# Kernel optimization log

Measured on AMD Instinct MI355X. Metric: run time of the kernel, lower is better.

## Reference

```python
import jax, jax.numpy as jnp
import numpy as np

N = 50_000        # nodes
E = 1_600_000     # edges (avg degree 32)
H = 64            # hidden_channels
DEPTH = 3         # -> 2*DEPTH mid conv layers


def setup_inputs() -> dict:
    key = jax.random.key(0)
    ks = jax.random.split(key, 8)
    x = jax.random.normal(ks[0], (N, 1), dtype=jnp.float32)
    edge_index = jax.random.randint(ks[1], (2, E), 0, N, dtype=jnp.int32)
    s = 0.1  # small init scale
    W_in = s * jax.random.normal(ks[2], (2 * 1 + 1, H), dtype=jnp.float32)
    b_in = jnp.zeros((H,), jnp.float32)
    W_mid = s * jax.random.normal(ks[3], (2 * DEPTH, 2 * H + 1, H), dtype=jnp.float32)
    b_mid = jnp.zeros((2 * DEPTH, H), jnp.float32)
    W_out = s * jax.random.normal(ks[4], (2 * H + 1, 1), dtype=jnp.float32)
    b_out = jnp.zeros((1,), jnp.float32)
    return {"x": x, "edge_index": edge_index, "W_in": W_in, "b_in": b_in,
            "W_mid": W_mid, "b_mid": b_mid, "W_out": W_out, "b_out": b_out}


def _conv(x, src, dst, sign, inv_deg, W, b):
    """Directional_EdgeConv: mean_{j->i} Linear([x_i, x_j - x_i, sign(j-i)])."""
    x_i = x[dst]                                   # [E, F] target feats
    x_j = x[src]                                   # [E, F] source feats
    feat = jnp.concatenate([x_i, x_j - x_i, sign], axis=-1)  # [E, 2F+1]
    msg = feat @ W + b                             # [E, out]
    agg = jax.ops.segment_sum(msg, dst, num_segments=x.shape[0])  # [N, out]
    return agg * inv_deg                           # mean aggregation


def reference(x, edge_index, W_in, b_in, W_mid, b_mid, W_out, b_out):
    src = edge_index[0]
    dst = edge_index[1]
    # vectorized replacement of the per-edge Python sign loop
    sign = jnp.sign((src - dst).astype(x.dtype))[:, None]        # [E, 1]
    deg = jax.ops.segment_sum(jnp.ones((src.shape[0],), x.dtype), dst,
                              num_segments=x.shape[0])
    inv_deg = (1.0 / jnp.maximum(deg, 1.0))[:, None]             # [N, 1]

    x2 = _conv(x, src, dst, sign, inv_deg, W_in, b_in)
    for l in range(DEPTH):
        x1 = jax.nn.leaky_relu(
            _conv(x2, src, dst, sign, inv_deg, W_mid[2 * l], b_mid[2 * l]))
        x2 = jax.nn.leaky_relu(
            _conv(x1, src, dst, sign, inv_deg, W_mid[2 * l + 1], b_mid[2 * l + 1]) + x2)
    return _conv(x2, src, dst, sign, inv_deg, W_out, b_out) + x
```

## Files before the change

kernel.cpp:

```cpp
#include <hip/hip_runtime.h>
#include <hip/hip_fp16.h>

#define HDIM 64
#define NEG_SLOPE 0.01f
#define CAPB 8192
#define BCAP 6144

typedef _Float16 half8 __attribute__((ext_vector_type(8)));
typedef float f32x4 __attribute__((ext_vector_type(4)));

static __device__ __forceinline__ float h_lo(unsigned d) {
    return __half2float(__ushort_as_half((unsigned short)(d & 0xffffu)));
}
static __device__ __forceinline__ float h_hi(unsigned d) {
    return __half2float(__ushort_as_half((unsigned short)(d >> 16)));
}
static __device__ __forceinline__ unsigned packh(float a, float b) {
    unsigned short ra = __half_as_ushort(__float2half(a));
    unsigned short rb = __half_as_ushort(__float2half(b));
    return ((unsigned)rb << 16) | (unsigned)ra;
}
static __device__ __forceinline__ half8 u4h(uint4 v) {
    union { uint4 u; half8 h; } x; x.u = v; return x.h;
}
static __device__ __forceinline__ __half2 uh2(unsigned u) {
    union { unsigned u; __half2 h; } x; x.u = u; return x.h;
}
static __device__ __forceinline__ unsigned h2u(__half2 h) {
    union { __half2 h; unsigned u; } x; x.h = h; return x.u;
}
static __device__ __forceinline__ __half2 hsum8(unsigned a, unsigned b, unsigned c, unsigned d,
                                                unsigned e, unsigned f, unsigned g, unsigned h) {
    __half2 p0 = __hadd2(uh2(a), uh2(b));
    __half2 p1 = __hadd2(uh2(c), uh2(d));
    __half2 p2 = __hadd2(uh2(e), uh2(f));
    __half2 p3 = __hadd2(uh2(g), uh2(h));
    return __hadd2(__hadd2(p0, p1), __hadd2(p2, p3));
}

__global__ void k_setup(int ptotal, const float* __restrict__ W_mid,
                        unsigned short* __restrict__ WTh,
                        int NB, int* gcur, int N, unsigned* xAP, unsigned* xBP) {
    int i = blockIdx.x * blockDim.x + threadIdx.x;
    if (i < ptotal) {
        int l = i >> 13;
        int rem = i & 8191;
        int h = rem >> 7;
        int k = rem & 127;
        const float* W = W_mid + (size_t)l * 129 * 64;
        float v = W[k * 64 + h] - ((k < 64) ? W[(64 + k) * 64 + h] : 0.f);
        WTh[i] = __half_as_ushort(__float2half(v));
    }
    if (i < NB) gcur[i] = i * CAPB;
    if (i < 32) xAP[(size_t)N * 32 + i] = 0u;
    else if (i < 64) xBP[(size_t)N * 32 + (i - 32)] = 0u;
}

__global__ void k_bucket(int E, const int* __restrict__ src, const int* __restrict__ dst,
                         int* gcur, unsigned* __restrict__ bucketed, int NB) {
    __shared__ int lh[512];
    __shared__ int lbase[512];
    int t = threadIdx.x;
    int e0 = blockIdx.x * 2048;
    for (int i = t; i < NB; i += 256) lh[i] = 0;
    __syncthreads();
    int dv[8];
#pragma unroll
    for (int k = 0; k < 8; ++k) {
        int e = e0 + k * 256 + t;
        dv[k] = (e < E) ? dst[e] : -1;
    }
#pragma unroll
    for (int k = 0; k < 8; ++k)
        if (dv[k] >= 0) atomicAdd(&lh[((unsigned)dv[k]) >> 7], 1);
    __syncthreads();
    for (int i = t; i < NB; i += 256) {
        int c = lh[i];
        lbase[i] = (c > 0) ? atomicAdd(&gcur[i], c) : 0;
        lh[i] = 0;
    }
    __syncthreads();
    int sv[8];
#pragma unroll
    for (int k = 0; k < 8; ++k) {
        int e = e0 + k * 256 + t;
        sv[k] = (e < E) ? src[e] : 0;
    }
#pragma unroll
    for (int k = 0; k < 8; ++k) {
        if (dv[k] >= 0) {
            int b = ((unsigned)dv[k]) >> 7;
            int r = atomicAdd(&lh[b], 1);
            int pos = lbase[b] + r;
            if (pos < (b + 1) * CAPB)
                bucketed[pos] = ((unsigned)dv[k] << 16) | (unsigned)sv[k];
        }
    }
}

__global__ void k_bktscan(int NB, int N, const int* __restrict__ gcur,
                          int* gstart, int* rowptr) {
    __shared__ int sd[512];
    int t = threadIdx.x;
    int c = (t < NB) ? min(gcur[t] - t * CAPB, CAPB) : 0;
    sd[t] = c;
    __syncthreads();
    int x = c;
    for (int s = 1; s < 512; s <<= 1) {
        int p = (t >= s) ? sd[t - s] : 0;
        __syncthreads();
        x += p;
        sd[t] = x;
        __syncthreads();
    }
    if (t < NB) gstart[t] = x - c;
    if (t == NB - 1) {
        gstart[NB] = x;
        rowptr[N] = x;
    }
}

__global__ void k_csr(int N, const unsigned* __restrict__ bucketed, const int* __restrict__ gcur,
                      const int* __restrict__ gstart, unsigned short* __restrict__ csr,
                      unsigned short* __restrict__ pcsr,
                      int* __restrict__ rowptr, float* __restrict__ ssinv) {
    __shared__ unsigned st[BCAP];
    __shared__ int hist[128], cur[128], excl[128], sgp[128];
    int b = blockIdx.x, t = threadIdx.x;
    int n0 = b << 7;
    int nn = min(128, N - n0);
    int cnt = min(gcur[b] - b * CAPB, CAPB);
    int base = gstart[b];
    if (t < 128) { hist[t] = 0; sgp[t] = 0; }
    unsigned sent = ((unsigned)N << 16) | (unsigned)N;
    unsigned* pb32 = (unsigned*)(pcsr + ((size_t)b << 13));
    for (int i = t; i < 4096; i += 256) pb32[i] = sent;
    __syncthreads();
    bool single = (cnt <= BCAP);
    for (int off = 0; off < cnt; off += BCAP) {
        int bs = min(BCAP, cnt - off);
        for (int i = t; i < bs; i += 256) {
            unsigned w = bucketed[b * CAPB + off + i];
            if (single) st[i] = w;
            int d = (int)(w >> 16);
            int s = (int)(w & 0xffffu);
            int dl = d - n0;
            atomicAdd(&hist[dl], 1);
            atomicAdd(&sgp[dl], ((s < d) ? 1024 : 0) + ((s == d) ? 1 : 0));
        }
    }
    __syncthreads();
    int deg_t = (t < 128) ? hist[t] : 0;
    int x = deg_t;
    for (int s = 1; s < 128; s <<= 1) {
        int p = (t < 128 && t >= s) ? hist[t - s] : 0;
        __syncthreads();
        if (t < 128) { x += p; hist[t] = x; }
        __syncthreads();
    }
    if (t < 128) {
        int ex = hist[t] - deg_t;
        excl[t] = ex;
        cur[t] = ex;
        if (t < nn) {
            rowptr[n0 + t] = base + ex;
            int sg = sgp[t];
            int lt = sg >> 10, eq = sg & 1023;
            float ss = (float)(deg_t - eq - 2 * lt);
            ssinv[n0 + t] = (deg_t > 0) ? ss / (float)deg_t : 0.f;
        }
    }
    __syncthreads();
    for (int off = 0; off < cnt; off += BCAP) {
        int bs = min(BCAP, cnt - off);
        if (!single) {
            for (int i = t; i < bs; i += 256) st[i] = bucketed[b * CAPB + off + i];
            __syncthreads();
        }
        for (int i = t; i < bs; i += 256) {
            unsigned w = st[i];
            int dl = (int)(w >> 16) - n0;
            unsigned short sval = (unsigned short)(w & 0xffffu);
            int p = atomicAdd(&cur[dl], 1);
            csr[base + p] = sval;
            int r = p - excl[dl];
            if (r < 64) pcsr[((size_t)(n0 + dl) << 6) + r] = sval;
        }
        if (!single) __syncthreads();
    }
}

__global__ void k_in(int N, const float* __restrict__ x0,
                     const int* __restrict__ rowptr, const unsigned short* __restrict__ csr,
                     const float* __restrict__ ssinv,
                     const float* __restrict__ W_in, const float* __restrict__ b_in,
                     unsigned* __restrict__ xoutP) {
    int wid = blockIdx.x * (blockDim.x >> 6) + (threadIdx.x >> 6);
    int lane = threadIdx.x & 63;
    if (wid >= N) return;
    int beg = rowptr[wid], end = rowptr[wid + 1];
    int deg = end - beg;
    float s = 0.f;
    for (int e = beg + lane; e < end; e += 64) s += x0[csr[e]];
    for (int m = 32; m >= 1; m >>= 1) s += __shfl_xor(s, m, 64);
    float invd = 1.f / (float)max(deg, 1);
    float mean = s * invd;
    float xi = x0[wid];
    float w1 = W_in[lane], w2 = W_in[64 + lane], w3 = W_in[128 + lane];
    float y = xi * (w1 - w2) + mean * w2 + ssinv[wid] * w3 + b_in[lane];
    if (deg == 0) y = 0.f;
    float ylo = __shfl(y, (2 * lane) & 63, 64);
    float yhi = __shfl(y, (2 * lane + 1) & 63, 64);
    unsigned pkd = packh(ylo, yhi);
    if (lane < 32) xoutP[(size_t)wid * 32 + lane] = pkd;
}

static __device__ __forceinline__ void slow_gather(
        const uint4* __restrict__ xin16, const unsigned short* __restrict__ csr,
        int beg, int end, int N, int lane, int sub, int lq, float* a) {
#pragma unroll
    for (int j = 0; j < 8; ++j) a[j] = 0.f;
    for (int tb = beg; tb < end; tb += 64) {
        int cnt = min(64, end - tb);
        int sv = (lane < cnt) ? (int)csr[tb + lane] : N;
        int ng = (cnt + 7) >> 3;
        for (int g = 0; g < ng; ++g) {
            int si = __shfl(sv, (g << 3) + sub, 64);
            uint4 d = xin16[(size_t)si * 8 + lq];
            a[0] += h_lo(d.x); a[1] += h_hi(d.x);
            a[2] += h_lo(d.y); a[3] += h_hi(d.y);
            a[4] += h_lo(d.z); a[5] += h_hi(d.z);
            a[6] += h_lo(d.w); a[7] += h_hi(d.w);
        }
    }
#pragma unroll
    for (int m = 8; m <= 32; m <<= 1) {
#pragma unroll
        for (int j = 0; j < 8; ++j) a[j] += __shfl_xor(a[j], m, 64);
    }
}

template <bool RES>
__global__ __launch_bounds__(256) void k_layer(
        int N, const unsigned* __restrict__ xinP,
        const unsigned* __restrict__ xresP, unsigned* __restrict__ xoutP,
        const int* __restrict__ rowptr, const unsigned short* __restrict__ csr,
        const unsigned short* __restrict__ pcsr,
        const float* __restrict__ ssinv,
        const unsigned short* __restrict__ WThl,
        const float* __restrict__ W3, const float* __restrict__ bias) {
    __shared__ unsigned Ald[16 * 64];
    __shared__ float Cld[16 * 64];
    __shared__ int sdeg[16];
    __shared__ float sss[16];

    int t = threadIdx.x;
    int lane = t & 63;
    int wv = t >> 6;
    int n0 = blockIdx.x << 4;
    int kg = lane >> 4;

    int cb = (wv << 4) + (lane & 15);
    const uint4* wp = (const uint4*)WThl;
    uint4 b0 = wp[cb * 16 + kg + 0];
    uint4 b1 = wp[cb * 16 + kg + 4];
    uint4 b2 = wp[cb * 16 + kg + 8];
    uint4 b3 = wp[cb * 16 + kg + 12];

    const uint4* xin16 = (const uint4*)xinP;
    int sub = lane >> 3;
    int lq = lane & 7;
    int ndb = wv << 2;

    int svp[4];
#pragma unroll
    for (int q = 0; q < 4; ++q)
        svp[q] = (int)pcsr[((size_t)(n0 + ndb + q) << 6) + lane];

#pragma unroll
    for (int qp = 0; qp < 2; ++qp) {
        int ndA = ndb + (qp << 1);
        int ndB = ndA + 1;
        int nodeA = n0 + ndA, nodeB = n0 + ndB;
        int ncA = min(nodeA, N - 1), ncB = min(nodeB, N - 1);
        int begA = __builtin_amdgcn_readfirstlane(rowptr[ncA]);
        int endA = __builtin_amdgcn_readfirstlane(rowptr[ncA + 1]);
        int begB = __builtin_amdgcn_readfirstlane(rowptr[ncB]);
        int endB = __builtin_amdgcn_readfirstlane(rowptr[ncB + 1]);
        int degA = (nodeA < N) ? (endA - begA) : 0;
        int degB = (nodeB < N) ? (endB - begB) : 0;
        float ssvA = ssinv[ncA];
        float ssvB = ssinv[ncB];
        uint4 xiA = make_uint4(0u, 0u, 0u, 0u), xiB = make_uint4(0u, 0u, 0u, 0u);
        if (lane < 8) {
            xiA = xin16[(size_t)ncA * 8 + lane];
            xiB = xin16[(size_t)ncB * 8 + lane];
        }
        uint4 mvA, mvB;
        if (max(degA, degB) <= 64) {
            int svA = svp[qp << 1], svB = svp[(qp << 1) + 1];
            int sA0 = __shfl(svA, sub, 64),      sB0 = __shfl(svB, sub, 64);
            int sA1 = __shfl(svA, 8 + sub, 64),  sB1 = __shfl(svB, 8 + sub, 64);
            int sA2 = __shfl(svA, 16 + sub, 64), sB2 = __shfl(svB, 16 + sub, 64);
            int sA3 = __shfl(svA, 24 + sub, 64), sB3 = __shfl(svB, 24 + sub, 64);
            int sA4 = __shfl(svA, 32 + sub, 64), sB4 = __shfl(svB, 32 + sub, 64);
            int sA5 = __shfl(svA, 40 + sub, 64), sB5 = __shfl(svB, 40 + sub, 64);
            int sA6 = __shfl(svA, 48 + sub, 64), sB6 = __shfl(svB, 48 + sub, 64);
            int sA7 = __shfl(svA, 56 + sub, 64), sB7 = __shfl(svB, 56 + sub, 64);
            uint4 dA0 = xin16[(size_t)sA0 * 8 + lq];
            uint4 dA1 = xin16[(size_t)sA1 * 8 + lq];
            uint4 dA2 = xin16[(size_t)sA2 * 8 + lq];
            uint4 dA3 = xin16[(size_t)sA3 * 8 + lq];
            uint4 dA4 = xin16[(size_t)sA4 * 8 + lq];
            uint4 dA5 = xin16[(size_t)sA5 * 8 + lq];
            uint4 dA6 = xin16[(size_t)sA6 * 8 + lq];
            uint4 dA7 = xin16[(size_t)sA7 * 8 + lq];
            uint4 dB0 = xin16[(size_t)sB0 * 8 + lq];
            uint4 dB1 = xin16[(size_t)sB1 * 8 + lq];
            uint4 dB2 = xin16[(size_t)sB2 * 8 + lq];
            uint4 dB3 = xin16[(size_t)sB3 * 8 + lq];
            uint4 dB4 = xin16[(size_t)sB4 * 8 + lq];
            uint4 dB5 = xin16[(size_t)sB5 * 8 + lq];
            uint4 dB6 = xin16[(size_t)sB6 * 8 + lq];
            uint4 dB7 = xin16[(size_t)sB7 * 8 + lq];
            unsigned uA0 = h2u(hsum8(dA0.x, dA1.x, dA2.x, dA3.x, dA4.x, dA5.x, dA6.x, dA7.x));
            unsigned uA1 = h2u(hsum8(dA0.y, dA1.y, dA2.y, dA3.y, dA4.y, dA5.y, dA6.y, dA7.y));
            unsigned uA2 = h2u(hsum8(dA0.z, dA1.z, dA2.z, dA3.z, dA4.z, dA5.z, dA6.z, dA7.z));
            unsigned uA3 = h2u(hsum8(dA0.w, dA1.w, dA2.w, dA3.w, dA4.w, dA5.w, dA6.w, dA7.w));
            unsigned uB0 = h2u(hsum8(dB0.x, dB1.x, dB2.x, dB3.x, dB4.x, dB5.x, dB6.x, dB7.x));
            unsigned uB1 = h2u(hsum8(dB0.y, dB1.y, dB2.y, dB3.y, dB4.y, dB5.y, dB6.y, dB7.y));
            unsigned uB2 = h2u(hsum8(dB0.z, dB1.z, dB2.z, dB3.z, dB4.z, dB5.z, dB6.z, dB7.z));
            unsigned uB3 = h2u(hsum8(dB0.w, dB1.w, dB2.w, dB3.w, dB4.w, dB5.w, dB6.w, dB7.w));
#pragma unroll
            for (int m = 8; m <= 32; m <<= 1) {
                uA0 = h2u(__hadd2(uh2(uA0), uh2((unsigned)__shfl_xor((int)uA0, m, 64))));
                uA1 = h2u(__hadd2(uh2(uA1), uh2((unsigned)__shfl_xor((int)uA1, m, 64))));
                uA2 = h2u(__hadd2(uh2(uA2), uh2((unsigned)__shfl_xor((int)uA2, m, 64))));
                uA3 = h2u(__hadd2(uh2(uA3), uh2((unsigned)__shfl_xor((int)uA3, m, 64))));
                uB0 = h2u(__hadd2(uh2(uB0), uh2((unsigned)__shfl_xor((int)uB0, m, 64))));
                uB1 = h2u(__hadd2(uh2(uB1), uh2((unsigned)__shfl_xor((int)uB1, m, 64))));
                uB2 = h2u(__hadd2(uh2(uB2), uh2((unsigned)__shfl_xor((int)uB2, m, 64))));
                uB3 = h2u(__hadd2(uh2(uB3), uh2((unsigned)__shfl_xor((int)uB3, m, 64))));
            }
            float idA = 1.f / (float)max(degA, 1);
            float idB = 1.f / (float)max(degB, 1);
            mvA.x = packh(__half2float(__low2half(uh2(uA0))) * idA, __half2float(__high2half(uh2(uA0))) * idA);
            mvA.y = packh(__half2float(__low2half(uh2(uA1))) * idA, __half2float(__high2half(uh2(uA1))) * idA);
            mvA.z = packh(__half2float(__low2half(uh2(uA2))) * idA, __half2float(__high2half(uh2(uA2))) * idA);
            mvA.w = packh(__half2float(__low2half(uh2(uA3))) * idA, __half2float(__high2half(uh2(uA3))) * idA);
            mvB.x = packh(__half2float(__low2half(uh2(uB0))) * idB, __half2float(__high2half(uh2(uB0))) * idB);
            mvB.y = packh(__half2float(__low2half(uh2(uB1))) * idB, __half2float(__high2half(uh2(uB1))) * idB);
            mvB.z = packh(__half2float(__low2half(uh2(uB2))) * idB, __half2float(__high2half(uh2(uB2))) * idB);
            mvB.w = packh(__half2float(__low2half(uh2(uB3))) * idB, __half2float(__high2half(uh2(uB3))) * idB);
        } else {
            float aA[8], aB[8];
            slow_gather(xin16, csr, begA, endA, N, lane, sub, lq, aA);
            slow_gather(xin16, csr, begB, endB, N, lane, sub, lq, aB);
            float idA = 1.f / (float)max(degA, 1);
            float idB = 1.f / (float)max(degB, 1);
            mvA.x = packh(aA[0] * idA, aA[1] * idA);
            mvA.y = packh(aA[2] * idA, aA[3] * idA);
            mvA.z = packh(aA[4] * idA, aA[5] * idA);
            mvA.w = packh(aA[6] * idA, aA[7] * idA);
            mvB.x = packh(aB[0] * idB, aB[1] * idB);
            mvB.y = packh(aB[2] * idB, aB[3] * idB);
            mvB.z = packh(aB[4] * idB, aB[5] * idB);
            mvB.w = packh(aB[6] * idB, aB[7] * idB);
        }
        if (lane < 8) {
            int gxA = lane ^ (ndA & 7), gmA = (8 + lane) ^ (ndA & 7);
            int gxB = lane ^ (ndB & 7), gmB = (8 + lane) ^ (ndB & 7);
            ((uint4*)Ald)[ndA * 16 + gxA] = xiA;
            ((uint4*)Ald)[ndA * 16 + gmA] = mvA;
            ((uint4*)Ald)[ndB * 16 + gxB] = xiB;
            ((uint4*)Ald)[ndB * 16 + gmB] = mvB;
        }
        if (lane == 0) {
            sdeg[ndA] = degA; sss[ndA] = ssvA;
            sdeg[ndB] = degB; sss[ndB] = ssvB;
        }
    }
    __syncthreads();

    int r = lane & 15;
    const uint4* ap = (const uint4*)Ald;
    int rx = (r & 7);
    uint4 fa0 = ap[r * 16 + ((0 + kg) ^ rx)];
    uint4 fa1 = ap[r * 16 + ((4 + kg) ^ rx)];
    uint4 fa2 = ap[r * 16 + ((8 + kg) ^ rx)];
    uint4 fa3 = ap[r * 16 + ((12 + kg) ^ rx)];
    f32x4 acc = {0.f, 0.f, 0.f, 0.f};
    acc = __builtin_amdgcn_mfma_f32_16x16x32_f16(u4h(fa0), u4h(b0), acc, 0, 0, 0);
    acc = __builtin_amdgcn_mfma_f32_16x16x32_f16(u4h(fa1), u4h(b1), acc, 0, 0, 0);
    acc = __builtin_amdgcn_mfma_f32_16x16x32_f16(u4h(fa2), u4h(b2), acc, 0, 0, 0);
    acc = __builtin_amdgcn_mfma_f32_16x16x32_f16(u4h(fa3), u4h(b3), acc, 0, 0, 0);
#pragma unroll
    for (int reg = 0; reg < 4; ++reg)
        Cld[(kg * 4 + reg) * 64 + (wv << 4) + r] = acc[reg];
    __syncthreads();

    int nd = t >> 4;
    int node = n0 + nd;
    if (node < N) {
        int dg = sdeg[nd];
        float ss = sss[nd];
#pragma unroll
        for (int jj = 0; jj < 2; ++jj) {
            int j = (t & 15) + jj * 16;
            float y0 = Cld[nd * 64 + 2 * j];
            float y1 = Cld[nd * 64 + 2 * j + 1];
            float2 w3 = ((const float2*)W3)[j];
            float2 bb = ((const float2*)bias)[j];
            y0 += ss * w3.x + bb.x;
            y1 += ss * w3.y + bb.y;
            if (dg == 0) { y0 = 0.f; y1 = 0.f; }
            if (RES) {
                unsigned rw = xresP[(size_t)node * 32 + j];
                y0 += h_lo(rw);
                y1 += h_hi(rw);
            }
            y0 = (y0 > 0.f) ? y0 : NEG_SLOPE * y0;
            y1 = (y1 > 0.f) ? y1 : NEG_SLOPE * y1;
            xoutP[(size_t)node * 32 + j] = packh(y0, y1);
        }
    }
}

__global__ void k_t(int N, const unsigned* __restrict__ xAP, const float* __restrict__ Wt,
                    float* __restrict__ t) {
    int wid = blockIdx.x * (blockDim.x >> 6) + (threadIdx.x >> 6);
    int lane = threadIdx.x & 63;
    if (wid >= N) return;
    float p = 0.f;
    if (lane < 32) {
        unsigned d = xAP[(size_t)wid * 32 + lane];
        float2 wt = ((const float2*)Wt)[lane];
        p = h_lo(d) * wt.x + h_hi(d) * wt.y;
    }
    for (int m = 32; m >= 1; m >>= 1) p += __shfl_xor(p, m, 64);
    if (lane == 0) t[wid] = p;
}

__global__ void k_out(int N, const unsigned* __restrict__ xAP, const float* __restrict__ x0,
                      const int* __restrict__ rowptr, const unsigned short* __restrict__ csr,
                      const float* __restrict__ ssinv, const float* __restrict__ t,
                      const float* __restrict__ W_out, const float* __restrict__ b_out,
                      float* __restrict__ out) {
    int wid = blockIdx.x * (blockDim.x >> 6) + (threadIdx.x >> 6);
    int lane = threadIdx.x & 63;
    if (wid >= N) return;
    int beg = rowptr[wid], end = rowptr[wid + 1];
    int deg = end - beg;
    float s = 0.f;
    for (int e = beg + lane; e < end; e += 64) s += t[csr[e]];
    unsigned xw = xAP[(size_t)wid * 32 + (lane >> 1)];
    float xf = (lane & 1) ? h_hi(xw) : h_lo(xw);
    float p = xf * (W_out[lane] - W_out[64 + lane]);
    for (int m = 32; m >= 1; m >>= 1) {
        s += __shfl_xor(s, m, 64);
        p += __shfl_xor(p, m, 64);
    }
    float invd = 1.f / (float)max(deg, 1);
    float y = p + s * invd + ssinv[wid] * W_out[128] + b_out[0];
    if (deg == 0) y = 0.f;
    if (lane == 0) out[wid] = y + x0[wid];
}

static inline size_t align16(size_t x) { return (x + 15) & ~(size_t)15; }

extern "C" void kernel_launch(void* const* d_in, const int* in_sizes, int n_in,
                              void* d_out, int out_size, void* d_ws, size_t ws_size,
                              hipStream_t stream) {
    const float* x0    = (const float*)d_in[0];
    const int*   ei    = (const int*)d_in[1];
    const float* W_in  = (const float*)d_in[2];
    const float* b_in  = (const float*)d_in[3];
    const float* W_mid = (const float*)d_in[4];
    const float* b_mid = (const float*)d_in[5];
    const float* W_out = (const float*)d_in[6];
    const float* b_out = (const float*)d_in[7];
    float* out = (float*)d_out;

    const int N = in_sizes[0];
    const int E = in_sizes[1] / 2;
    const int L = in_sizes[4] / (129 * 64);
    const int NB = (N + 127) >> 7;
    const int* src = ei;
    const int* dst = ei + E;

    char* p = (char*)d_ws;
    unsigned short* WTh = (unsigned short*)p; p += align16((size_t)L * 64 * 128 * 2);
    unsigned* xAP = (unsigned*)p; p += align16((size_t)(N + 1) * 32 * 4);
    unsigned* xBP = (unsigned*)p; p += align16((size_t)(N + 1) * 32 * 4);
    unsigned* bucketed = (unsigned*)p; p += align16((size_t)NB * CAPB * 4);
    unsigned short* csr = (unsigned short*)p; p += align16((size_t)E * 2);
    unsigned short* pcsr = (unsigned short*)p; p += align16((size_t)NB * 8192 * 2);
    int* gcur          = (int*)p; p += align16((size_t)(NB + 1) * 4);
    int* gstart        = (int*)p; p += align16((size_t)(NB + 1) * 4);
    int* rowptr        = (int*)p; p += align16((size_t)(N + 1) * 4);
    float* ssinv       = (float*)p; p += align16((size_t)N * 4);
    float* t           = (float*)p; p += align16((size_t)N * 4);

    const int nb_w4 = (N + 3) / 4;
    const int nb_bkt = (E + 2047) / 2048;
    const int ptotal = L * 64 * 128;
    const int nb_lay = (N + 15) / 16;

    k_setup<<<(ptotal + 255) / 256, 256, 0, stream>>>(ptotal, W_mid, WTh, NB, gcur, N, xAP, xBP);
    k_bucket<<<nb_bkt, 256, 0, stream>>>(E, src, dst, gcur, bucketed, NB);
    k_bktscan<<<1, 512, 0, stream>>>(NB, N, gcur, gstart, rowptr);
    k_csr<<<NB, 256, 0, stream>>>(N, bucketed, gcur, gstart, csr, pcsr, rowptr, ssinv);

    k_in<<<nb_w4, 256, 0, stream>>>(N, x0, rowptr, csr, ssinv, W_in, b_in, xAP);

    for (int l = 0; l < L / 2; ++l) {
        const unsigned short* Wa = WTh + (size_t)(2 * l) * 64 * 128;
        const unsigned short* Wb = WTh + (size_t)(2 * l + 1) * 64 * 128;
        const float* W3a = W_mid + (size_t)(2 * l) * 129 * 64 + 128 * 64;
        const float* W3b = W_mid + (size_t)(2 * l + 1) * 129 * 64 + 128 * 64;

        k_layer<false><<<nb_lay, 256, 0, stream>>>(
            N, xAP, nullptr, xBP, rowptr, csr, pcsr, ssinv,
            Wa, W3a, b_mid + (size_t)(2 * l) * HDIM);
        k_layer<true><<<nb_lay, 256, 0, stream>>>(
            N, xBP, xAP, xAP, rowptr, csr, pcsr, ssinv,
            Wb, W3b, b_mid + (size_t)(2 * l + 1) * HDIM);
    }

    k_t<<<nb_w4, 256, 0, stream>>>(N, xAP, W_out + 64, t);
    k_out<<<nb_w4, 256, 0, stream>>>(N, xAP, x0, rowptr, csr, ssinv, t,
                                     W_out, b_out, out);
}
```

Before: 270.3 us.

## Fuse output projection into last layer, skip unused gather chunk, widen bucket blocks

The final layer kernel now computes the per-node dot product with W_out directly from its fp32 outputs and writes t, which removes the separate k_t kernel and its re-read of xAP. The fast gather path for nodes with degree at most 64 now loads the second 32-neighbour chunk only when the degree exceeds 32, avoiding padded loads for low-degree nodes. It also accumulates in half2 registers through a helper. k_bucket moves from 256 to 1024 threads per block with two edges per thread. The new t is computed from unrounded fp32 values instead of fp16-stored ones, so the output changes slightly.

```diff
diff --git a/kernel.cpp b/kernel.cpp
--- a/kernel.cpp
+++ b/kernel.cpp
@@ -25,17 +25,6 @@
 }
 static __device__ __forceinline__ __half2 uh2(unsigned u) {
     union { unsigned u; __half2 h; } x; x.u = u; return x.h;
-}
-static __device__ __forceinline__ unsigned h2u(__half2 h) {
-    union { __half2 h; unsigned u; } x; x.h = h; return x.u;
-}
-static __device__ __forceinline__ __half2 hsum8(unsigned a, unsigned b, unsigned c, unsigned d,
-                                                unsigned e, unsigned f, unsigned g, unsigned h) {
-    __half2 p0 = __hadd2(uh2(a), uh2(b));
-    __half2 p1 = __hadd2(uh2(c), uh2(d));
-    __half2 p2 = __hadd2(uh2(e), uh2(f));
-    __half2 p3 = __hadd2(uh2(g), uh2(h));
-    return __hadd2(__hadd2(p0, p1), __hadd2(p2, p3));
 }
 
 __global__ void k_setup(int ptotal, const float* __restrict__ W_mid,
@@ -56,45 +45,42 @@
     else if (i < 64) xBP[(size_t)N * 32 + (i - 32)] = 0u;
 }
 
-__global__ void k_bucket(int E, const int* __restrict__ src, const int* __restrict__ dst,
-                         int* gcur, unsigned* __restrict__ bucketed, int NB) {
+__global__ __launch_bounds__(1024) void k_bucket(
+        int E, const int* __restrict__ src, const int* __restrict__ dst,
+        int* gcur, unsigned* __restrict__ bucketed, int NB) {
     __shared__ int lh[512];
     __shared__ int lbase[512];
     int t = threadIdx.x;
     int e0 = blockIdx.x * 2048;
-    for (int i = t; i < NB; i += 256) lh[i] = 0;
-    __syncthreads();
-    int dv[8];
-#pragma unroll
-    for (int k = 0; k < 8; ++k) {
-        int e = e0 + k * 256 + t;
-        dv[k] = (e < E) ? dst[e] : -1;
-    }
-#pragma unroll
-    for (int k = 0; k < 8; ++k)
-        if (dv[k] >= 0) atomicAdd(&lh[((unsigned)dv[k]) >> 7], 1);
-    __syncthreads();
-    for (int i = t; i < NB; i += 256) {
-        int c = lh[i];
-        lbase[i] = (c > 0) ? atomicAdd(&gcur[i], c) : 0;
-        lh[i] = 0;
-    }
-    __syncthreads();
-    int sv[8];
-#pragma unroll
-    for (int k = 0; k < 8; ++k) {
-        int e = e0 + k * 256 + t;
-        sv[k] = (e < E) ? src[e] : 0;
-    }
-#pragma unroll
-    for (int k = 0; k < 8; ++k) {
-        if (dv[k] >= 0) {
-            int b = ((unsigned)dv[k]) >> 7;
-            int r = atomicAdd(&lh[b], 1);
-            int pos = lbase[b] + r;
-            if (pos < (b + 1) * CAPB)
-                bucketed[pos] = ((unsigned)dv[k] << 16) | (unsigned)sv[k];
-        }
+    if (t < 512) lh[t] = 0;
+    __syncthreads();
+    int e1 = e0 + t, e2 = e0 + 1024 + t;
+    int d1 = (e1 < E) ? dst[e1] : -1;
+    int d2 = (e2 < E) ? dst[e2] : -1;
+    if (d1 >= 0) atomicAdd(&lh[((unsigned)d1) >> 7], 1);
+    if (d2 >= 0) atomicAdd(&lh[((unsigned)d2) >> 7], 1);
+    __syncthreads();
+    if (t < NB) {
+        int c = lh[t];
+        lbase[t] = (c > 0) ? atomicAdd(&gcur[t], c) : 0;
+        lh[t] = 0;
+    }
+    __syncthreads();
+    int s1 = (e1 < E) ? src[e1] : 0;
+    int s2 = (e2 < E) ? src[e2] : 0;
+    if (d1 >= 0) {
+        int b = ((unsigned)d1) >> 7;
+        int r = atomicAdd(&lh[b], 1);
+        int pos = lbase[b] + r;
+        if (pos < (b + 1) * CAPB)
+            bucketed[pos] = ((unsigned)d1 << 16) | (unsigned)s1;
+    }
+    if (d2 >= 0) {
+        int b = ((unsigned)d2) >> 7;
+        int r = atomicAdd(&lh[b], 1);
+        int pos = lbase[b] + r;
+        if (pos < (b + 1) * CAPB)
+            bucketed[pos] = ((unsigned)d2 << 16) | (unsigned)s2;
     }
 }
 
@@ -215,6 +201,23 @@
     if (lane < 32) xoutP[(size_t)wid * 32 + lane] = pkd;
 }
 
+static __device__ __forceinline__ void chunk_acc(
+        const uint4* __restrict__ xin16, int sv, int base, int sub, int lq,
+        __half2& c0, __half2& c1, __half2& c2, __half2& c3) {
+    int s0 = __shfl(sv, base + sub, 64);
+    int s1 = __shfl(sv, base + 8 + sub, 64);
+    int s2 = __shfl(sv, base + 16 + sub, 64);
+    int s3 = __shfl(sv, base + 24 + sub, 64);
+    uint4 d0 = xin16[(size_t)s0 * 8 + lq];
+    uint4 d1 = xin16[(size_t)s1 * 8 + lq];
+    uint4 d2 = xin16[(size_t)s2 * 8 + lq];
+    uint4 d3 = xin16[(size_t)s3 * 8 + lq];
+    c0 = __hadd2(c0, __hadd2(__hadd2(uh2(d0.x), uh2(d1.x)), __hadd2(uh2(d2.x), uh2(d3.x))));
+    c1 = __hadd2(c1, __hadd2(__hadd2(uh2(d0.y), uh2(d1.y)), __hadd2(uh2(d2.y), uh2(d3.y))));
+    c2 = __hadd2(c2, __hadd2(__hadd2(uh2(d0.z), uh2(d1.z)), __hadd2(uh2(d2.z), uh2(d3.z))));
+    c3 = __hadd2(c3, __hadd2(__hadd2(uh2(d0.w), uh2(d1.w)), __hadd2(uh2(d2.w), uh2(d3.w))));
+}
+
 static __device__ __forceinline__ void slow_gather(
         const uint4* __restrict__ xin16, const unsigned short* __restrict__ csr,
         int beg, int end, int N, int lane, int sub, int lq, float* a) {
@@ -240,7 +243,7 @@
     }
 }
 
-template <bool RES>
+template <bool RES, bool TOUT>
 __global__ __launch_bounds__(256) void k_layer(
         int N, const unsigned* __restrict__ xinP,
         const unsigned* __restrict__ xresP, unsigned* __restrict__ xoutP,
@@ -248,7 +251,8 @@
         const unsigned short* __restrict__ pcsr,
         const float* __restrict__ ssinv,
         const unsigned short* __restrict__ WThl,
-        const float* __restrict__ W3, const float* __restrict__ bias) {
+        const float* __restrict__ W3, const float* __restrict__ bias,
+        const float* __restrict__ Wt, float* __restrict__ tvec) {
     __shared__ unsigned Ald[16 * 64];
     __shared__ float Cld[16 * 64];
     __shared__ int sdeg[16];
@@ -298,60 +302,35 @@
         }
         uint4 mvA, mvB;
         if (max(degA, degB) <= 64) {
+            __half2 z = uh2(0u);
+            __half2 cA0 = z, cA1 = z, cA2 = z, cA3 = z;
+            __half2 cB0 = z, cB1 = z, cB2 = z, cB3 = z;
             int svA = svp[qp << 1], svB = svp[(qp << 1) + 1];
-            int sA0 = __shfl(svA, sub, 64),      sB0 = __shfl(svB, sub, 64);
-            int sA1 = __shfl(svA, 8 + sub, 64),  sB1 = __shfl(svB, 8 + sub, 64);
-            int sA2 = __shfl(svA, 16 + sub, 64), sB2 = __shfl(svB, 16 + sub, 64);
-            int sA3 = __shfl(svA, 24 + sub, 64), sB3 = __shfl(svB, 24 + sub, 64);
-            int sA4 = __shfl(svA, 32 + sub, 64), sB4 = __shfl(svB, 32 + sub, 64);
-            int sA5 = __shfl(svA, 40 + sub, 64), sB5 = __shfl(svB, 40 + sub, 64);
-            int sA6 = __shfl(svA, 48 + sub, 64), sB6 = __shfl(svB, 48 + sub, 64);
-            int sA7 = __shfl(svA, 56 + sub, 64), sB7 = __shfl(svB, 56 + sub, 64);
-            uint4 dA0 = xin16[(size_t)sA0 * 8 + lq];
-            uint4 dA1 = xin16[(size_t)sA1 * 8 + lq];
-            uint4 dA2 = xin16[(size_t)sA2 * 8 + lq];
-            uint4 dA3 = xin16[(size_t)sA3 * 8 + lq];
-            uint4 dA4 = xin16[(size_t)sA4 * 8 + lq];
-            uint4 dA5 = xin16[(size_t)sA5 * 8 + lq];
-            uint4 dA6 = xin16[(size_t)sA6 * 8 + lq];
-            uint4 dA7 = xin16[(size_t)sA7 * 8 + lq];
-            uint4 dB0 = xin16[(size_t)sB0 * 8 + lq];
-            uint4 dB1 = xin16[(size_t)sB1 * 8 + lq];
-            uint4 dB2 = xin16[(size_t)sB2 * 8 + lq];
-            uint4 dB3 = xin16[(size_t)sB3 * 8 + lq];
-            uint4 dB4 = xin16[(size_t)sB4 * 8 + lq];
-            uint4 dB5 = xin16[(size_t)sB5 * 8 + lq];
-            uint4 dB6 = xin16[(size_t)sB6 * 8 + lq];
-            uint4 dB7 = xin16[(size_t)sB7 * 8 + lq];
-            unsigned uA0 = h2u(hsum8(dA0.x, dA1.x, dA2.x, dA3.x, dA4.x, dA5.x, dA6.x, dA7.x));
-            unsigned uA1 = h2u(hsum8(dA0.y, dA1.y, dA2.y, dA3.y, dA4.y, dA5.y, dA6.y, dA7.y));
-            unsigned uA2 = h2u(hsum8(dA0.z, dA1.z, dA2.z, dA3.z, dA4.z, dA5.z, dA6.z, dA7.z));
-            unsigned uA3 = h2u(hsum8(dA0.w, dA1.w, dA2.w, dA3.w, dA4.w, dA5.w, dA6.w, dA7.w));
-            unsigned uB0 = h2u(hsum8(dB0.x, dB1.x, dB2.x, dB3.x, dB4.x, dB5.x, dB6.x, dB7.x));
-            unsigned uB1 = h2u(hsum8(dB0.y, dB1.y, dB2.y, dB3.y, dB4.y, dB5.y, dB6.y, dB7.y));
-            unsigned uB2 = h2u(hsum8(dB0.z, dB1.z, dB2.z, dB3.z, dB4.z, dB5.z, dB6.z, dB7.z));
-            unsigned uB3 = h2u(hsum8(dB0.w, dB1.w, dB2.w, dB3.w, dB4.w, dB5.w, dB6.w, dB7.w));
+            chunk_acc(xin16, svA, 0, sub, lq, cA0, cA1, cA2, cA3);
+            chunk_acc(xin16, svB, 0, sub, lq, cB0, cB1, cB2, cB3);
+            if (degA > 32) chunk_acc(xin16, svA, 32, sub, lq, cA0, cA1, cA2, cA3);
+            if (degB > 32) chunk_acc(xin16, svB, 32, sub, lq, cB0, cB1, cB2, cB3);
 #pragma unroll
             for (int m = 8; m <= 32; m <<= 1) {
-                uA0 = h2u(__hadd2(uh2(uA0), uh2((unsigned)__shfl_xor((int)uA0, m, 64))));
-                uA1 = h2u(__hadd2(uh2(uA1), uh2((unsigned)__shfl_xor((int)uA1, m, 64))));
-                uA2 = h2u(__hadd2(uh2(uA2), uh2((unsigned)__shfl_xor((int)uA2, m, 64))));
-                uA3 = h2u(__hadd2(uh2(uA3), uh2((unsigned)__shfl_xor((int)uA3, m, 64))));
-                uB0 = h2u(__hadd2(uh2(uB0), uh2((unsigned)__shfl_xor((int)uB0, m, 64))));
-                uB1 = h2u(__hadd2(uh2(uB1), uh2((unsigned)__shfl_xor((int)uB1, m, 64))));
-                uB2 = h2u(__hadd2(uh2(uB2), uh2((unsigned)__shfl_xor((int)uB2, m, 64))));
-                uB3 = h2u(__hadd2(uh2(uB3), uh2((unsigned)__shfl_xor((int)uB3, m, 64))));
+                cA0 = __hadd2(cA0, uh2((unsigned)__shfl_xor((int)*(unsigned*)&cA0, m, 64)));
+                cA1 = __hadd2(cA1, uh2((unsigned)__shfl_xor((int)*(unsigned*)&cA1, m, 64)));
+                cA2 = __hadd2(cA2, uh2((unsigned)__shfl_xor((int)*(unsigned*)&cA2, m, 64)));
+                cA3 = __hadd2(cA3, uh2((unsigned)__shfl_xor((int)*(unsigned*)&cA3, m, 64)));
+                cB0 = __hadd2(cB0, uh2((unsigned)__shfl_xor((int)*(unsigned*)&cB0, m, 64)));
+                cB1 = __hadd2(cB1, uh2((unsigned)__shfl_xor((int)*(unsigned*)&cB1, m, 64)));
+                cB2 = __hadd2(cB2, uh2((unsigned)__shfl_xor((int)*(unsigned*)&cB2, m, 64)));
+                cB3 = __hadd2(cB3, uh2((unsigned)__shfl_xor((int)*(unsigned*)&cB3, m, 64)));
             }
             float idA = 1.f / (float)max(degA, 1);
             float idB = 1.f / (float)max(degB, 1);
-            mvA.x = packh(__half2float(__low2half(uh2(uA0))) * idA, __half2float(__high2half(uh2(uA0))) * idA);
-            mvA.y = packh(__half2float(__low2half(uh2(uA1))) * idA, __half2float(__high2half(uh2(uA1))) * idA);
-            mvA.z = packh(__half2float(__low2half(uh2(uA2))) * idA, __half2float(__high2half(uh2(uA2))) * idA);
-            mvA.w = packh(__half2float(__low2half(uh2(uA3))) * idA, __half2float(__high2half(uh2(uA3))) * idA);
-            mvB.x = packh(__half2float(__low2half(uh2(uB0))) * idB, __half2float(__high2half(uh2(uB0))) * idB);
-            mvB.y = packh(__half2float(__low2half(uh2(uB1))) * idB, __half2float(__high2half(uh2(uB1))) * idB);
-            mvB.z = packh(__half2float(__low2half(uh2(uB2))) * idB, __half2float(__high2half(uh2(uB2))) * idB);
-            mvB.w = packh(__half2float(__low2half(uh2(uB3))) * idB, __half2float(__high2half(uh2(uB3))) * idB);
+            mvA.x = packh(__half2float(__low2half(cA0)) * idA, __half2float(__high2half(cA0)) * idA);
+            mvA.y = packh(__half2float(__low2half(cA1)) * idA, __half2float(__high2half(cA1)) * idA);
+            mvA.z = packh(__half2float(__low2half(cA2)) * idA, __half2float(__high2half(cA2)) * idA);
+            mvA.w = packh(__half2float(__low2half(cA3)) * idA, __half2float(__high2half(cA3)) * idA);
+            mvB.x = packh(__half2float(__low2half(cB0)) * idB, __half2float(__high2half(cB0)) * idB);
+            mvB.y = packh(__half2float(__low2half(cB1)) * idB, __half2float(__high2half(cB1)) * idB);
+            mvB.z = packh(__half2float(__low2half(cB2)) * idB, __half2float(__high2half(cB2)) * idB);
+            mvB.w = packh(__half2float(__low2half(cB3)) * idB, __half2float(__high2half(cB3)) * idB);
         } else {
             float aA[8], aB[8];
             slow_gather(xin16, csr, begA, endA, N, lane, sub, lq, aA);
@@ -404,6 +383,7 @@
     if (node < N) {
         int dg = sdeg[nd];
         float ss = sss[nd];
+        float tp = 0.f;
 #pragma unroll
         for (int jj = 0; jj < 2; ++jj) {
             int j = (t & 15) + jj * 16;
@@ -421,24 +401,20 @@
             }
             y0 = (y0 > 0.f) ? y0 : NEG_SLOPE * y0;
             y1 = (y1 > 0.f) ? y1 : NEG_SLOPE * y1;
+            if (TOUT) {
+                float2 wt = ((const float2*)Wt)[j];
+                tp += y0 * wt.x + y1 * wt.y;
+            }
             xoutP[(size_t)node * 32 + j] = packh(y0, y1);
         }
-    }
-}
-
-__global__ void k_t(int N, const unsigned* __restrict__ xAP, const float* __restrict__ Wt,
-                    float* __restrict__ t) {
-    int wid = blockIdx.x * (blockDim.x >> 6) + (threadIdx.x >> 6);
-    int lane = threadIdx.x & 63;
-    if (wid >= N) return;
-    float p = 0.f;
-    if (lane < 32) {
-        unsigned d = xAP[(size_t)wid * 32 + lane];
-        float2 wt = ((const float2*)Wt)[lane];
-        p = h_lo(d) * wt.x + h_hi(d) * wt.y;
-    }
-    for (int m = 32; m >= 1; m >>= 1) p += __shfl_xor(p, m, 64);
-    if (lane == 0) t[wid] = p;
+        if (TOUT) {
+            tp += __shfl_xor(tp, 1, 64);
+            tp += __shfl_xor(tp, 2, 64);
+            tp += __shfl_xor(tp, 4, 64);
+            tp += __shfl_xor(tp, 8, 64);
+            if ((t & 15) == 0) tvec[node] = tp;
+        }
+    }
 }
 
 __global__ void k_out(int N, const unsigned* __restrict__ xAP, const float* __restrict__ x0,
@@ -507,27 +483,33 @@
     const int nb_lay = (N + 15) / 16;
 
     k_setup<<<(ptotal + 255) / 256, 256, 0, stream>>>(ptotal, W_mid, WTh, NB, gcur, N, xAP, xBP);
-    k_bucket<<<nb_bkt, 256, 0, stream>>>(E, src, dst, gcur, bucketed, NB);
+    k_bucket<<<nb_bkt, 1024, 0, stream>>>(E, src, dst, gcur, bucketed, NB);
     k_bktscan<<<1, 512, 0, stream>>>(NB, N, gcur, gstart, rowptr);
     k_csr<<<NB, 256, 0, stream>>>(N, bucketed, gcur, gstart, csr, pcsr, rowptr, ssinv);
 
     k_in<<<nb_w4, 256, 0, stream>>>(N, x0, rowptr, csr, ssinv, W_in, b_in, xAP);
 
     for (int l = 0; l < L / 2; ++l) {
+        bool last = (l == L / 2 - 1);
         const unsigned short* Wa = WTh + (size_t)(2 * l) * 64 * 128;
         const unsigned short* Wb = WTh + (size_t)(2 * l + 1) * 64 * 128;
         const float* W3a = W_mid + (size_t)(2 * l) * 129 * 64 + 128 * 64;
         const float* W3b = W_mid + (size_t)(2 * l + 1) * 129 * 64 + 128 * 64;
 
-        k_layer<false><<<nb_lay, 256, 0, stream>>>(
+        k_layer<false, false><<<nb_lay, 256, 0, stream>>>(
             N, xAP, nullptr, xBP, rowptr, csr, pcsr, ssinv,
-            Wa, W3a, b_mid + (size_t)(2 * l) * HDIM);
-        k_layer<true><<<nb_lay, 256, 0, stream>>>(
-            N, xBP, xAP, xAP, rowptr, csr, pcsr, ssinv,
-            Wb, W3b, b_mid + (size_t)(2 * l + 1) * HDIM);
-    }
-
-    k_t<<<nb_w4, 256, 0, stream>>>(N, xAP, W_out + 64, t);
+            Wa, W3a, b_mid + (size_t)(2 * l) * HDIM, nullptr, nullptr);
+        if (!last) {
+            k_layer<true, false><<<nb_lay, 256, 0, stream>>>(
+                N, xBP, xAP, xAP, rowptr, csr, pcsr, ssinv,
+                Wb, W3b, b_mid + (size_t)(2 * l + 1) * HDIM, nullptr, nullptr);
+        } else {
+            k_layer<true, true><<<nb_lay, 256, 0, stream>>>(
+                N, xBP, xAP, xAP, rowptr, csr, pcsr, ssinv,
+                Wb, W3b, b_mid + (size_t)(2 * l + 1) * HDIM, W_out + 64, t);
+        }
+    }
+
     k_out<<<nb_w4, 256, 0, stream>>>(N, xAP, x0, rowptr, csr, ssinv, t,
                                      W_out, b_out, out);
 }
```

Result: faster. 254.7 us (-5.8%).
